# Kernel tuning notes

Measured on AMD Instinct MI355X. Metric: run time of the kernel, lower is better.

The kernel has to match this reference:

```python
import jax, jax.numpy as jnp
import numpy as np

B, S, D, H = 2, 2048, 1024, 16
HD = D // H  # head_dim = 64


def setup_inputs() -> dict:
    key = jax.random.key(0)
    k1, k2, k3 = jax.random.split(key, 3)
    x = jax.random.normal(k1, (B, S, D), dtype=jnp.float32)
    W_attn = jax.random.normal(k2, (3 * D, D), dtype=jnp.float32) * (D ** -0.5)
    W_proj = jax.random.normal(k3, (D, D), dtype=jnp.float32) * (D ** -0.5)
    b_proj = jnp.zeros((D,), dtype=jnp.float32)
    return {"x": x, "W_attn": W_attn, "W_proj": W_proj, "b_proj": b_proj}


def reference(x, W_attn, W_proj, b_proj):
    b, s, d = x.shape
    h, hd = H, d // H
    # fused QKV projection (torch Linear: x @ W^T), then split
    qkv = jnp.einsum('bsd,ed->bse', x, W_attn)  # [B,S,3D]
    q, k, v = jnp.split(qkv, 3, axis=-1)
    # [B,S,D] -> [B,H,S,hd]
    q = q.reshape(b, s, h, hd).transpose(0, 2, 1, 3)
    k = k.reshape(b, s, h, hd).transpose(0, 2, 1, 3)
    v = v.reshape(b, s, h, hd).transpose(0, 2, 1, 3)
    # manual softmax attention (no causal mask in the non-flash branch)
    att = jnp.einsum('bhqd,bhkd->bhqk', q, k) * (1.0 / jnp.sqrt(jnp.float32(hd)))
    att = jax.nn.softmax(att, axis=-1)  # attn_dropout is identity in eval
    y = jnp.einsum('bhqk,bhkd->bhqd', att, v)
    y = y.transpose(0, 2, 1, 3).reshape(b, s, d)
    y = jnp.einsum('bsd,ed->bse', y, W_proj) + b_proj  # resid_dropout identity
    return y, att
```

## Files before the change

kernel.cpp:

```cpp
#include <hip/hip_runtime.h>

typedef _Float16 f16;
typedef f16 f16x4 __attribute__((ext_vector_type(4)));
typedef f16 f16x8 __attribute__((ext_vector_type(8)));
typedef float f32x4 __attribute__((ext_vector_type(4)));
typedef unsigned int u32;
typedef unsigned long long u64;

#define DEV static __device__ __forceinline__

#define S_ 2048
#define D_ 1024

#define S_WAITV(n) asm volatile("s_waitcnt vmcnt(" #n ") lgkmcnt(0)" ::: "memory")

DEV int swz64(int row, int chunk) { return row * 64 + (((chunk ^ row) & 7) << 3); }

DEV void gload16(const void* g, void* l) {
    __builtin_amdgcn_global_load_lds((const __attribute__((address_space(1))) u32*)g,
                                     (__attribute__((address_space(3))) u32*)l, 16, 0, 0);
}
DEV float exp2_fast(float x) { float r; asm("v_exp_f32 %0, %1" : "=v"(r) : "v"(x)); return r; }

__global__ void convert_f16(const float* __restrict__ x, const float* __restrict__ wa,
                            const float* __restrict__ wp,
                            f16* __restrict__ xb, f16* __restrict__ wab, f16* __restrict__ wpb) {
    u32 t = blockIdx.x * blockDim.x + threadIdx.x;
    u32 base = t * 8u;
    const float* src; f16* dst; u32 off;
    if (base < 4194304u)      { src = x;  dst = xb;  off = base; }
    else if (base < 7340032u) { src = wa; dst = wab; off = base - 4194304u; }
    else                      { src = wp; dst = wpb; off = base - 7340032u; }
    float4 a = *(const float4*)(src + off);
    float4 b = *(const float4*)(src + off + 4);
    f16x8 v;
    v[0] = (f16)a.x; v[1] = (f16)a.y; v[2] = (f16)a.z; v[3] = (f16)a.w;
    v[4] = (f16)b.x; v[5] = (f16)b.y; v[6] = (f16)b.z; v[7] = (f16)b.w;
    *(f16x8*)(dst + off) = v;
}

template <int EPI>
__global__ __launch_bounds__(256) void gemm_bt(
    const f16* __restrict__ A, const f16* __restrict__ Bt, int K,
    f16* __restrict__ oQ, f16* __restrict__ oK, f16* __restrict__ oV,
    float* __restrict__ oY, const float* __restrict__ bias) {
    __shared__ f16 smem[3][8192];
    f16* sm = &smem[0][0];
    const int tid = threadIdx.x;
    const int lane = tid & 63;
    const int la = lane & 15, lg = lane >> 4;
    const int wv = tid >> 6;
    const int wr = (wv >> 1) << 6, wc = (wv & 1) << 6;
    const int r0 = blockIdx.x << 7, c0 = blockIdx.y << 7;

    const f32x4 VZ = {0.f, 0.f, 0.f, 0.f};
    f32x4 acc[4][4];
#pragma unroll
    for (int m = 0; m < 4; ++m)
#pragma unroll
        for (int n = 0; n < 4; ++n) acc[m][n] = VZ;

    const int srow = tid >> 2, scol = (tid & 3) << 3;
    const f16* Ag = A + (u64)(r0 + srow) * K + scol;
    const f16* Bg = Bt + (u64)(c0 + srow) * K + scol;
    const u64 K64 = (u64)K << 6;

    const int NT = K >> 5;
#define STAGE(k0, slot)                                              \
    do {                                                             \
        f16* Al = smem[slot] + wv * 512;                             \
        f16* Bl = smem[slot] + 4096 + wv * 512;                      \
        gload16(Ag + (k0), Al);                                      \
        gload16(Ag + K64 + (k0), Al + 2048);                         \
        gload16(Bg + (k0), Bl);                                      \
        gload16(Bg + K64 + (k0), Bl + 2048);                         \
    } while (0)

    STAGE(0, 0);
    STAGE(32, 1);
    S_WAITV(4);
    __builtin_amdgcn_s_barrier();

    for (int t = 0; t < NT; ++t) {
        if (t > 0) {
            if (t < NT - 1) { S_WAITV(4); } else { S_WAITV(0); }
            __builtin_amdgcn_s_barrier();
        }
        if (t + 2 < NT) STAGE((t + 2) << 5, (t + 2) % 3);
        const f16* As = smem[t % 3];
        const f16* Bs = smem[t % 3] + 4096;
        f16x8 af[4], bf[4];
#pragma unroll
        for (int m = 0; m < 4; ++m) af[m] = *(const f16x8*)(As + (wr + m * 16 + la) * 32 + lg * 8);
#pragma unroll
        for (int n = 0; n < 4; ++n) bf[n] = *(const f16x8*)(Bs + (wc + n * 16 + la) * 32 + lg * 8);
#pragma unroll
        for (int m = 0; m < 4; ++m)
#pragma unroll
            for (int n = 0; n < 4; ++n)
                acc[m][n] = __builtin_amdgcn_mfma_f32_16x16x32_f16(af[m], bf[n], acc[m][n], 0, 0, 0);
    }
#undef STAGE

    if (EPI == 0) {
        if (c0 < 2048) {
#pragma unroll
            for (int n = 0; n < 4; ++n) {
                int col = c0 + wc + n * 16 + la;
#pragma unroll
                for (int m = 0; m < 4; ++m) {
#pragma unroll
                    for (int j = 0; j < 4; ++j) {
                        int row = r0 + wr + m * 16 + lg * 4 + j;
                        int b = row >> 11, s = row & 2047;
                        float val = acc[m][n][j];
                        if (col < 1024) {
                            int h = col >> 6, hd = col & 63;
                            oQ[(((u64)(b * 16 + h)) * 2048 + s) * 64 + hd] = (f16)(val * 0.18033688f);
                        } else {
                            int d = col - 1024, h = d >> 6, hd = d & 63;
                            oK[(((u64)(b * 16 + h)) * 2048 + s) * 64 + hd] = (f16)val;
                        }
                    }
                }
            }
        } else {
            const int hbase = (c0 - 2048) >> 6;
            const int b = r0 >> 11, sb = r0 & 2047;
#pragma unroll
            for (int hh = 0; hh < 2; ++hh) {
                __syncthreads();
                if ((wv & 1) == hh) {
#pragma unroll
                    for (int n = 0; n < 4; ++n) {
                        int hd = n * 16 + la;
#pragma unroll
                        for (int m = 0; m < 4; ++m) {
                            int s = wr + m * 16 + lg * 4;
                            int pos = (s & ~31) | (lg << 3) | (((s >> 4) & 1) << 2);
                            f16x4 pk;
                            pk[0] = (f16)acc[m][n][0]; pk[1] = (f16)acc[m][n][1];
                            pk[2] = (f16)acc[m][n][2]; pk[3] = (f16)acc[m][n][3];
                            *(f16x4*)(sm + hd * 136 + pos) = pk;
                        }
                    }
                }
                __syncthreads();
                {
                    int hd = tid >> 2, qtr = tid & 3;
                    f16* dst = oV + (((u64)(b * 16 + hbase + hh)) * 64 + hd) * 2048 + sb + qtr * 32;
#pragma unroll
                    for (int i = 0; i < 4; ++i)
                        *(f16x8*)(dst + i * 8) = *(const f16x8*)(sm + hd * 136 + qtr * 32 + i * 8);
                }
            }
        }
    } else {
#pragma unroll
        for (int n = 0; n < 4; ++n) {
            int col = c0 + wc + n * 16 + la;
            float bv = bias[col];
#pragma unroll
            for (int m = 0; m < 4; ++m)
#pragma unroll
                for (int j = 0; j < 4; ++j) {
                    int row = r0 + wr + m * 16 + lg * 4 + j;
                    oY[(u64)row * 1024 + col] = acc[m][n][j] + bv;
                }
        }
    }
}

__global__ __launch_bounds__(256) void attn_fused(
    const f16* __restrict__ q, const f16* __restrict__ k, const f16* __restrict__ vt,
    float* __restrict__ att, f16* __restrict__ ya) {
    __shared__ f16 smem[5 * 4096];
    f16* qs = smem + 4 * 4096;

    const int tid = threadIdx.x, lane = tid & 63, wv = tid >> 6;
    const int la = lane & 15, lg = lane >> 4;
    const int bh = blockIdx.x, qt = blockIdx.y;
    const f16* qh = q + (u64)bh * (S_ * 64) + qt * (64 * 64);
    const f16* kh = k + (u64)bh * (S_ * 64);
    const f16* vh = vt + (u64)bh * (S_ * 64);

    const int sr0 = wv * 8 + (lane >> 3);
    const int sr1 = sr0 + 32;
    const int sc0 = (((lane & 7) ^ (sr0 & 7)) << 3);
    const int sc1 = (((lane & 7) ^ (sr1 & 7)) << 3);
    const u64 go0 = (u64)sr0 * 64 + sc0, go1 = (u64)sr1 * 64 + sc1;
    const u64 gv0 = (u64)sr0 * 2048 + sc0, gv1 = (u64)sr1 * 2048 + sc1;

    gload16(qh + go0, qs + wv * 512);
    gload16(qh + go1, qs + 2048 + wv * 512);
    gload16(kh + go0, smem + wv * 512);
    gload16(kh + go1, smem + 2048 + wv * 512);
    gload16(kh + 4096 + go0, smem + 4096 + wv * 512);
    gload16(kh + 4096 + go1, smem + 4096 + 2048 + wv * 512);
    S_WAITV(2);
    __builtin_amdgcn_s_barrier();

    f16x8 qf[2];
    qf[0] = *(const f16x8*)(qs + swz64(wv * 16 + la, lg));
    qf[1] = *(const f16x8*)(qs + swz64(wv * 16 + la, 4 + lg));

    const f32x4 VZ = {0.f, 0.f, 0.f, 0.f};
    float psum = 0.f;

    for (int kt = 0; kt < 32; ++kt) {
        if (kt > 0) {
            if (kt < 31) { S_WAITV(2); } else { S_WAITV(0); }
            __builtin_amdgcn_s_barrier();
        }
        if (kt < 30) {
            const f16* kb = kh + (kt + 2) * 4096;
            f16* dst = smem + ((kt + 2) % 3) * 4096;
            gload16(kb + go0, dst + wv * 512);
            gload16(kb + go1, dst + 2048 + wv * 512);
        }
        const f16* kcur = smem + (kt % 3) * 4096;
        f32x4 sc[4] = {VZ, VZ, VZ, VZ};
#pragma unroll
        for (int ch = 0; ch < 2; ++ch)
#pragma unroll
            for (int n = 0; n < 4; ++n) {
                f16x8 kf = *(const f16x8*)(kcur + swz64(n * 16 + la, ch * 4 + lg));
                sc[n] = __builtin_amdgcn_mfma_f32_16x16x32_f16(kf, qf[ch], sc[n], 0, 0, 0);
            }
#pragma unroll
        for (int n = 0; n < 4; ++n)
#pragma unroll
            for (int j = 0; j < 4; ++j) psum += exp2_fast(sc[n][j]);
    }
    S_WAITV(0);
    __builtin_amdgcn_s_barrier();

    psum += __shfl_xor(psum, 16);
    psum += __shfl_xor(psum, 32);
    const float invl = 1.0f / psum;

    gload16(kh + go0, smem + wv * 512);
    gload16(kh + go1, smem + 2048 + wv * 512);
    gload16(vh + gv0, smem + 2 * 4096 + wv * 512);
    gload16(vh + gv1, smem + 2 * 4096 + 2048 + wv * 512);
    S_WAITV(0);
    __builtin_amdgcn_s_barrier();

    f32x4 accy[4] = {VZ, VZ, VZ, VZ};
    float* ab = att + ((u64)bh * S_ + (u64)qt * 64 + wv * 16 + la) * S_ + (lg << 2);
    for (int kt = 0; kt < 32; ++kt) {
        if (kt > 0) {
            S_WAITV(4);
            __builtin_amdgcn_s_barrier();
        }
        if (kt < 31) {
            const f16* kb = kh + (kt + 1) * 4096;
            const f16* vb = vh + (kt + 1) * 64;
            f16* kd = smem + ((kt + 1) & 1) * 4096;
            f16* vd = smem + (2 + ((kt + 1) & 1)) * 4096;
            gload16(kb + go0, kd + wv * 512);
            gload16(kb + go1, kd + 2048 + wv * 512);
            gload16(vb + gv0, vd + wv * 512);
            gload16(vb + gv1, vd + 2048 + wv * 512);
        }
        const f16* kcur = smem + (kt & 1) * 4096;
        const f16* vcur = smem + (2 + (kt & 1)) * 4096;

        f32x4 sc[4] = {VZ, VZ, VZ, VZ};
#pragma unroll
        for (int ch = 0; ch < 2; ++ch)
#pragma unroll
            for (int n = 0; n < 4; ++n) {
                f16x8 kf = *(const f16x8*)(kcur + swz64(n * 16 + la, ch * 4 + lg));
                sc[n] = __builtin_amdgcn_mfma_f32_16x16x32_f16(kf, qf[ch], sc[n], 0, 0, 0);
            }
        f32x4 pp[4];
#pragma unroll
        for (int n = 0; n < 4; ++n) {
#pragma unroll
            for (int j = 0; j < 4; ++j) pp[n][j] = exp2_fast(sc[n][j]) * invl;
            *(f32x4*)(ab + kt * 64 + n * 16) = pp[n];
        }
        f16x8 pa0, pa1;
#pragma unroll
        for (int j = 0; j < 4; ++j) {
            pa0[j] = (f16)pp[0][j]; pa0[j + 4] = (f16)pp[1][j];
            pa1[j] = (f16)pp[2][j]; pa1[j + 4] = (f16)pp[3][j];
        }
#pragma unroll
        for (int n = 0; n < 4; ++n) {
            f16x8 vf0 = *(const f16x8*)(vcur + swz64(n * 16 + la, lg));
            accy[n] = __builtin_amdgcn_mfma_f32_16x16x32_f16(pa0, vf0, accy[n], 0, 0, 0);
            f16x8 vf1 = *(const f16x8*)(vcur + swz64(n * 16 + la, 4 + lg));
            accy[n] = __builtin_amdgcn_mfma_f32_16x16x32_f16(pa1, vf1, accy[n], 0, 0, 0);
        }
    }

    const int b = bh >> 4, h = bh & 15;
    f16* yb = ya + ((u64)b * S_ + qt * 64 + wv * 16) * D_ + h * 64;
#pragma unroll
    for (int n = 0; n < 4; ++n)
#pragma unroll
        for (int j = 0; j < 4; ++j)
            yb[(u64)(lg * 4 + j) * D_ + n * 16 + la] = (f16)accy[n][j];
}

extern "C" void kernel_launch(void* const* d_in, const int* in_sizes, int n_in,
                              void* d_out, int out_size, void* d_ws, size_t ws_size,
                              hipStream_t stream) {
    const float* x  = (const float*)d_in[0];
    const float* wa = (const float*)d_in[1];
    const float* wp = (const float*)d_in[2];
    const float* bp = (const float*)d_in[3];
    float* outY   = (float*)d_out;
    float* outAtt = outY + 4194304ull;

    char* ws = (char*)d_ws;
    f16* xb  = (f16*)(ws + 0);
    f16* wab = (f16*)(ws + 8388608);
    f16* wpb = (f16*)(ws + 14680064);
    f16* qb  = (f16*)(ws + 16777216);
    f16* kb  = (f16*)(ws + 25165824);
    f16* vtb = (f16*)(ws + 33554432);
    f16* yab = (f16*)(ws + 41943040);

    convert_f16<<<4096, 256, 0, stream>>>(x, wa, wp, xb, wab, wpb);
    gemm_bt<0><<<dim3(32, 24), 256, 0, stream>>>(xb, wab, 1024, qb, kb, vtb, nullptr, nullptr);
    attn_fused<<<dim3(32, 32), 256, 0, stream>>>(qb, kb, vtb, outAtt, yab);
    gemm_bt<1><<<dim3(32, 8), 256, 0, stream>>>(yab, wpb, 1024, nullptr, nullptr, nullptr, outY, bp);
}
```

Before: 231.4 us.

## Split attention into single-wave blocks with private K/V pipelines, no barriers

The attention kernel moves from 256-thread blocks (4 waves sharing K/V tiles for 64 query rows) to 64-thread blocks that each handle 16 query rows. Each wave streams its own 32-key K and V tiles through a double buffer, so workgroup barriers are no longer needed. This adds occupancy and removes barrier stalls. In exchange, K/V reuse across waves is lost, so global and L2 traffic for K/V grows by 4x. It also issues more, smaller loads per step.

```diff
diff --git a/kernel.cpp b/kernel.cpp
--- a/kernel.cpp
+++ b/kernel.cpp
@@ -13,6 +13,8 @@
 #define D_ 1024
 
 #define S_WAITV(n) asm volatile("s_waitcnt vmcnt(" #n ") lgkmcnt(0)" ::: "memory")
+#define LGKM0_SB() do { asm volatile("s_waitcnt lgkmcnt(0)" ::: "memory"); \
+                        __builtin_amdgcn_sched_barrier(0); } while (0)
 
 DEV int swz64(int row, int chunk) { return row * 64 + (((chunk ^ row) & 7) << 3); }
 
@@ -171,133 +173,122 @@
     }
 }
 
-__global__ __launch_bounds__(256) void attn_fused(
+__global__ __launch_bounds__(64) void attn_fused(
     const f16* __restrict__ q, const f16* __restrict__ k, const f16* __restrict__ vt,
     float* __restrict__ att, f16* __restrict__ ya) {
-    __shared__ f16 smem[5 * 4096];
-    f16* qs = smem + 4 * 4096;
-
-    const int tid = threadIdx.x, lane = tid & 63, wv = tid >> 6;
+    __shared__ f16 smem[8192];
+
+    const int lane = threadIdx.x & 63;
     const int la = lane & 15, lg = lane >> 4;
-    const int bh = blockIdx.x, qt = blockIdx.y;
-    const f16* qh = q + (u64)bh * (S_ * 64) + qt * (64 * 64);
+    const int bh = blockIdx.x, qw = blockIdx.y;
+    const f16* qh = q + (u64)bh * (S_ * 64) + qw * (16 * 64);
     const f16* kh = k + (u64)bh * (S_ * 64);
     const f16* vh = vt + (u64)bh * (S_ * 64);
 
-    const int sr0 = wv * 8 + (lane >> 3);
-    const int sr1 = sr0 + 32;
-    const int sc0 = (((lane & 7) ^ (sr0 & 7)) << 3);
-    const int sc1 = (((lane & 7) ^ (sr1 & 7)) << 3);
-    const u64 go0 = (u64)sr0 * 64 + sc0, go1 = (u64)sr1 * 64 + sc1;
-    const u64 gv0 = (u64)sr0 * 2048 + sc0, gv1 = (u64)sr1 * 2048 + sc1;
-
-    gload16(qh + go0, qs + wv * 512);
-    gload16(qh + go1, qs + 2048 + wv * 512);
-    gload16(kh + go0, smem + wv * 512);
-    gload16(kh + go1, smem + 2048 + wv * 512);
-    gload16(kh + 4096 + go0, smem + 4096 + wv * 512);
-    gload16(kh + 4096 + go1, smem + 4096 + 2048 + wv * 512);
-    S_WAITV(2);
-    __builtin_amdgcn_s_barrier();
-
+    const int kr = lane >> 3;
+    const int kc = ((lane & 7) ^ kr) << 3;
+    const int vr = lane >> 2;
+    const int vc = ((lane & 3) ^ (vr & 3)) << 3;
+
+#define STK(kt, sl) do { const f16* kb_ = kh + (u64)(kt) * 2048;              \
+        f16* d_ = smem + (sl) * 2048;                                         \
+        gload16(kb_ + (u64)(0 * 8 + kr) * 64 + kc, d_);                       \
+        gload16(kb_ + (u64)(1 * 8 + kr) * 64 + kc, d_ + 512);                 \
+        gload16(kb_ + (u64)(2 * 8 + kr) * 64 + kc, d_ + 1024);                \
+        gload16(kb_ + (u64)(3 * 8 + kr) * 64 + kc, d_ + 1536); } while (0)
+#define STV(kt, sl) do { const f16* vb_ = vh + (u64)(kt) * 32 + vc;           \
+        f16* d_ = smem + 4096 + (sl) * 2048;                                  \
+        gload16(vb_ + (u64)(0 * 16 + vr) * 2048, d_);                         \
+        gload16(vb_ + (u64)(1 * 16 + vr) * 2048, d_ + 512);                   \
+        gload16(vb_ + (u64)(2 * 16 + vr) * 2048, d_ + 1024);                  \
+        gload16(vb_ + (u64)(3 * 16 + vr) * 2048, d_ + 1536); } while (0)
+
+    {
+        f16* qstage = smem + 4096;
+        gload16(qh + (u64)kr * 64 + kc, qstage);
+        gload16(qh + (u64)(8 + kr) * 64 + kc, qstage + 512);
+        S_WAITV(0);
+    }
     f16x8 qf[2];
-    qf[0] = *(const f16x8*)(qs + swz64(wv * 16 + la, lg));
-    qf[1] = *(const f16x8*)(qs + swz64(wv * 16 + la, 4 + lg));
+    qf[0] = *(const f16x8*)(smem + 4096 + swz64(la, lg));
+    qf[1] = *(const f16x8*)(smem + 4096 + swz64(la, 4 + lg));
+    LGKM0_SB();
 
     const f32x4 VZ = {0.f, 0.f, 0.f, 0.f};
     float psum = 0.f;
 
-    for (int kt = 0; kt < 32; ++kt) {
-        if (kt > 0) {
-            if (kt < 31) { S_WAITV(2); } else { S_WAITV(0); }
-            __builtin_amdgcn_s_barrier();
-        }
-        if (kt < 30) {
-            const f16* kb = kh + (kt + 2) * 4096;
-            f16* dst = smem + ((kt + 2) % 3) * 4096;
-            gload16(kb + go0, dst + wv * 512);
-            gload16(kb + go1, dst + 2048 + wv * 512);
-        }
-        const f16* kcur = smem + (kt % 3) * 4096;
-        f32x4 sc[4] = {VZ, VZ, VZ, VZ};
+    STK(0, 0);
+    STK(1, 1);
+    S_WAITV(4);
+    for (int kt = 0; kt < 64; ++kt) {
+        if (kt > 0) { if (kt < 63) { S_WAITV(4); } else { S_WAITV(0); } }
+        const f16* kcur = smem + (kt & 1) * 2048;
+        f32x4 sc[2] = {VZ, VZ};
 #pragma unroll
         for (int ch = 0; ch < 2; ++ch)
 #pragma unroll
-            for (int n = 0; n < 4; ++n) {
+            for (int n = 0; n < 2; ++n) {
                 f16x8 kf = *(const f16x8*)(kcur + swz64(n * 16 + la, ch * 4 + lg));
                 sc[n] = __builtin_amdgcn_mfma_f32_16x16x32_f16(kf, qf[ch], sc[n], 0, 0, 0);
             }
 #pragma unroll
-        for (int n = 0; n < 4; ++n)
+        for (int n = 0; n < 2; ++n)
 #pragma unroll
             for (int j = 0; j < 4; ++j) psum += exp2_fast(sc[n][j]);
-    }
-    S_WAITV(0);
-    __builtin_amdgcn_s_barrier();
-
+        if (kt < 62) {
+            LGKM0_SB();
+            STK(kt + 2, (kt & 1));
+        }
+    }
     psum += __shfl_xor(psum, 16);
     psum += __shfl_xor(psum, 32);
     const float invl = 1.0f / psum;
-
-    gload16(kh + go0, smem + wv * 512);
-    gload16(kh + go1, smem + 2048 + wv * 512);
-    gload16(vh + gv0, smem + 2 * 4096 + wv * 512);
-    gload16(vh + gv1, smem + 2 * 4096 + 2048 + wv * 512);
-    S_WAITV(0);
-    __builtin_amdgcn_s_barrier();
-
+    LGKM0_SB();
+
+    STK(0, 0); STV(0, 0);
+    STK(1, 1); STV(1, 1);
+    S_WAITV(8);
     f32x4 accy[4] = {VZ, VZ, VZ, VZ};
-    float* ab = att + ((u64)bh * S_ + (u64)qt * 64 + wv * 16 + la) * S_ + (lg << 2);
-    for (int kt = 0; kt < 32; ++kt) {
-        if (kt > 0) {
-            S_WAITV(4);
-            __builtin_amdgcn_s_barrier();
-        }
-        if (kt < 31) {
-            const f16* kb = kh + (kt + 1) * 4096;
-            const f16* vb = vh + (kt + 1) * 64;
-            f16* kd = smem + ((kt + 1) & 1) * 4096;
-            f16* vd = smem + (2 + ((kt + 1) & 1)) * 4096;
-            gload16(kb + go0, kd + wv * 512);
-            gload16(kb + go1, kd + 2048 + wv * 512);
-            gload16(vb + gv0, vd + wv * 512);
-            gload16(vb + gv1, vd + 2048 + wv * 512);
-        }
-        const f16* kcur = smem + (kt & 1) * 4096;
-        const f16* vcur = smem + (2 + (kt & 1)) * 4096;
-
-        f32x4 sc[4] = {VZ, VZ, VZ, VZ};
+    float* ab = att + ((u64)bh * S_ + (u64)qw * 16 + la) * S_ + (lg << 2);
+    for (int kt = 0; kt < 64; ++kt) {
+        if (kt > 0) { if (kt < 63) { S_WAITV(10); } else { S_WAITV(2); } }
+        const f16* kcur = smem + (kt & 1) * 2048;
+        const f16* vcur = smem + 4096 + (kt & 1) * 2048;
+
+        f32x4 sc[2] = {VZ, VZ};
 #pragma unroll
         for (int ch = 0; ch < 2; ++ch)
 #pragma unroll
-            for (int n = 0; n < 4; ++n) {
+            for (int n = 0; n < 2; ++n) {
                 f16x8 kf = *(const f16x8*)(kcur + swz64(n * 16 + la, ch * 4 + lg));
                 sc[n] = __builtin_amdgcn_mfma_f32_16x16x32_f16(kf, qf[ch], sc[n], 0, 0, 0);
             }
-        f32x4 pp[4];
+        f32x4 pp[2];
+#pragma unroll
+        for (int n = 0; n < 2; ++n) {
+#pragma unroll
+            for (int j = 0; j < 4; ++j) pp[n][j] = exp2_fast(sc[n][j]) * invl;
+            *(f32x4*)(ab + kt * 32 + n * 16) = pp[n];
+        }
+        f16x8 pa;
+#pragma unroll
+        for (int j = 0; j < 4; ++j) { pa[j] = (f16)pp[0][j]; pa[j + 4] = (f16)pp[1][j]; }
 #pragma unroll
         for (int n = 0; n < 4; ++n) {
-#pragma unroll
-            for (int j = 0; j < 4; ++j) pp[n][j] = exp2_fast(sc[n][j]) * invl;
-            *(f32x4*)(ab + kt * 64 + n * 16) = pp[n];
-        }
-        f16x8 pa0, pa1;
-#pragma unroll
-        for (int j = 0; j < 4; ++j) {
-            pa0[j] = (f16)pp[0][j]; pa0[j + 4] = (f16)pp[1][j];
-            pa1[j] = (f16)pp[2][j]; pa1[j + 4] = (f16)pp[3][j];
-        }
-#pragma unroll
-        for (int n = 0; n < 4; ++n) {
-            f16x8 vf0 = *(const f16x8*)(vcur + swz64(n * 16 + la, lg));
-            accy[n] = __builtin_amdgcn_mfma_f32_16x16x32_f16(pa0, vf0, accy[n], 0, 0, 0);
-            f16x8 vf1 = *(const f16x8*)(vcur + swz64(n * 16 + la, 4 + lg));
-            accy[n] = __builtin_amdgcn_mfma_f32_16x16x32_f16(pa1, vf1, accy[n], 0, 0, 0);
-        }
-    }
+            f16x8 vf = *(const f16x8*)(vcur + (n * 16 + la) * 32 + ((lg ^ (la & 3)) << 3));
+            accy[n] = __builtin_amdgcn_mfma_f32_16x16x32_f16(pa, vf, accy[n], 0, 0, 0);
+        }
+        if (kt < 62) {
+            LGKM0_SB();
+            STK(kt + 2, (kt & 1));
+            STV(kt + 2, (kt & 1));
+        }
+    }
+#undef STK
+#undef STV
 
     const int b = bh >> 4, h = bh & 15;
-    f16* yb = ya + ((u64)b * S_ + qt * 64 + wv * 16) * D_ + h * 64;
+    f16* yb = ya + ((u64)b * S_ + qw * 16) * D_ + h * 64;
 #pragma unroll
     for (int n = 0; n < 4; ++n)
 #pragma unroll
@@ -326,6 +317,6 @@
 
     convert_f16<<<4096, 256, 0, stream>>>(x, wa, wp, xb, wab, wpb);
     gemm_bt<0><<<dim3(32, 24), 256, 0, stream>>>(xb, wab, 1024, qb, kb, vtb, nullptr, nullptr);
-    attn_fused<<<dim3(32, 32), 256, 0, stream>>>(qb, kb, vtb, outAtt, yab);
+    attn_fused<<<dim3(32, 128), 64, 0, stream>>>(qb, kb, vtb, outAtt, yab);
     gemm_bt<1><<<dim3(32, 8), 256, 0, stream>>>(yab, wpb, 1024, nullptr, nullptr, nullptr, outY, bp);
 }
```

New measurement: 276.8 us. 1.2x slower.
